# Optimization experiments

Hardware: AMD Instinct MI355X
Metric: run time of the kernel (lower is better)

Reference implementation:

```python
import jax, jax.numpy as jnp
import numpy as np

B, S, D, H, NL = 4, 1024, 512, 8, 2
DFF = 4 * D
EPS = 1e-5


def _layernorm(x, g, b):
    m = x.mean(-1, keepdims=True)
    v = ((x - m) ** 2).mean(-1, keepdims=True)
    return (x - m) / jnp.sqrt(v + EPS) * g + b


def _forward(x, Wq, bq, Wk, bk, Wv, bv, Wo, bo, W1, b1, W2, b2, ln1_g, ln1_b, ln2_g, ln2_b):
    Bn, Sn, Dn = x.shape
    Nl, Hh = Wq.shape[0], Wq.shape[1]
    dk = Dn // Hh  # scaling uses dmodel//h even though heads are full-width (faithful to SDPA)
    for i in range(Nl):
        # per-head full-width projections: each head maps dmodel -> dmodel
        q = jnp.einsum('bsd,hed->bhse', x, Wq[i]) + bq[i][:, None, :]
        k = jnp.einsum('bsd,hed->bhse', x, Wk[i]) + bk[i][:, None, :]
        v = jnp.einsum('bsd,hed->bhse', x, Wv[i]) + bv[i][:, None, :]
        scores = jnp.einsum('bhse,bhte->bhst', q, k) / jnp.sqrt(jnp.asarray(dk, x.dtype))
        attn = jax.nn.softmax(scores, axis=-1)
        heads = jnp.einsum('bhst,bhte->bhse', attn, v)          # [B,H,S,D]
        cat = heads.transpose(0, 2, 1, 3).reshape(Bn, Sn, Hh * Dn)  # concat heads -> [B,S,H*D]
        mha_out = cat @ Wo[i].T + bo[i]
        x = _layernorm(x + mha_out, ln1_g[i], ln1_b[i])
        ff = jax.nn.relu(x @ W1[i].T + b1[i]) @ W2[i].T + b2[i]
        x = _layernorm(x + ff, ln2_g[i], ln2_b[i])
    return x


def setup_inputs() -> dict:
    key = jax.random.key(0)
    ks = jax.random.split(key, 12)
    def w(k, shape, fan_in):
        return (jax.random.normal(k, shape, jnp.float32) / np.sqrt(fan_in)).astype(jnp.float32)
    inp = {
        'x': jax.random.normal(ks[0], (B, S, D), jnp.float32),
        'Wq': w(ks[1], (NL, H, D, D), D), 'bq': jnp.zeros((NL, H, D), jnp.float32),
        'Wk': w(ks[2], (NL, H, D, D), D), 'bk': jnp.zeros((NL, H, D), jnp.float32),
        'Wv': w(ks[3], (NL, H, D, D), D), 'bv': jnp.zeros((NL, H, D), jnp.float32),
        'Wo': w(ks[4], (NL, D, H * D), H * D), 'bo': jnp.zeros((NL, D), jnp.float32),
        'W1': w(ks[5], (NL, DFF, D), D), 'b1': jnp.zeros((NL, DFF), jnp.float32),
        'W2': w(ks[6], (NL, D, DFF), DFF), 'b2': jnp.zeros((NL, D), jnp.float32),
        'ln1_g': jnp.ones((NL, D), jnp.float32), 'ln1_b': jnp.zeros((NL, D), jnp.float32),
        'ln2_g': jnp.ones((NL, D), jnp.float32), 'ln2_b': jnp.zeros((NL, D), jnp.float32),
    }
    return inp


def reference(x, Wq, bq, Wk, bk, Wv, bv, Wo, bo, W1, b1, W2, b2, ln1_g, ln1_b, ln2_g, ln2_b):
    return _forward(x, Wq, bq, Wk, bk, Wv, bv, Wo, bo, W1, b1, W2, b2, ln1_g, ln1_b, ln2_g, ln2_b)
```

## Files before the change

### kernel.cpp

```cpp
#include <hip/hip_runtime.h>
#include <cstdint>
#include <cstddef>

#define NB 4
#define NS 1024
#define ND 512
#define NH 8
#define NLAYER 2
#define NDFF 2048

typedef __attribute__((ext_vector_type(8))) short short8;
typedef __attribute__((ext_vector_type(4))) float f32x4;
typedef __attribute__((ext_vector_type(4))) unsigned short u16x4;
typedef unsigned short u16;
typedef long long ll;

__device__ __forceinline__ float b2f(u16 u) {
  union { unsigned int i; float f; } x; x.i = ((unsigned int)u) << 16; return x.f;
}
__device__ __forceinline__ u16 f2b(float f) {
  union { float f; unsigned int i; } x; x.f = f;
  return (u16)((x.i + 0x7FFF + ((x.i >> 16) & 1)) >> 16);
}

struct Zm { int div; ll hi, lo; };
__device__ __forceinline__ ll zoff(Zm m, int z) {
  return (ll)(z / m.div) * m.hi + (ll)(z % m.div) * m.lo;
}

enum { F_BF16 = 1, F_RELU = 2, F_BCOL = 4, F_BROW = 8, F_RESID = 16 };

__device__ __forceinline__ void load_lds16(const void* g, void* s) {
  __builtin_amdgcn_global_load_lds(
      (const __attribute__((address_space(1))) void*)(uintptr_t)g,
      (__attribute__((address_space(3))) void*)(uint32_t)(uintptr_t)s, 16, 0, 0);
}

#define MFMA16(d, a, b) \
  asm volatile("v_mfma_f32_16x16x32_bf16 %0, %1, %2, %0" : "+v"(d) : "v"(a), "v"(b))

__global__ void __launch_bounds__(512, 2)
gemm8(const u16* __restrict__ A, int lda, Zm za,
      const u16* __restrict__ Bw, int ldb, Zm zb,
      const u16* __restrict__ Bw2, const float* __restrict__ bias2, int zsplit,
      void* __restrict__ Cv, int ldc, Zm zc,
      const float* __restrict__ bias, Zm zbias,
      const float* __restrict__ resid,
      float scale, int K, int flags)
{
  __shared__ __align__(16) char smem[2][65536];

  const int gx = gridDim.x, gy = gridDim.y;
  int id = (blockIdx.z * gy + blockIdx.y) * gx + blockIdx.x;
  const int nwg = gx * gy * (int)gridDim.z;
  if ((nwg & 7) == 0) id = (id & 7) * (nwg >> 3) + (id >> 3);
  const int bx = id % gx;
  const int rest = id / gx;
  const int by = rest % gy;
  const int z0 = rest / gy;

  int zB = z0;
  const u16* Bsel = Bw;
  const float* bsel = bias;
  if (z0 >= zsplit) { Bsel = Bw2; bsel = bias2; zB = z0 - zsplit; }

  A    += zoff(za, z0);
  Bsel += zoff(zb, zB);

  const int bm = by * 256, bn = bx * 256;
  const int t = threadIdx.x;
  const int w = t >> 6, lane = t & 63;
  const int wr = w >> 2, wc = w & 3;

  const int swcol = (((t & 7) ^ ((t >> 3) & 7)) << 3);
  const u16* srcA = A    + (size_t)(bm + (t >> 3)) * lda + swcol;
  const u16* srcB = Bsel + (size_t)(bn + (t >> 3)) * ldb + swcol;
  char* const sbase = (char*)smem;
  const int wofs = w << 10;

  auto STAGE_A = [&](int kt) {
    const ll kofs = (ll)kt << 6;
    char* d0 = sbase + ((kt & 1) << 16);
#pragma unroll
    for (int h = 0; h < 2; ++h)
#pragma unroll
      for (int i = 0; i < 2; ++i)
        load_lds16(srcA + (size_t)(h * 128 + i * 64) * lda + kofs,
                   d0 + h * 16384 + i * 8192 + wofs);
  };
  auto STAGE_B = [&](int kt) {
    const ll kofs = (ll)kt << 6;
    char* d0 = sbase + ((kt & 1) << 16) + 32768;
#pragma unroll
    for (int h = 0; h < 2; ++h)
#pragma unroll
      for (int i = 0; i < 2; ++i)
        load_lds16(srcB + (size_t)(h * 128 + i * 64) * ldb + kofs,
                   d0 + h * 16384 + i * 8192 + wofs);
  };

  const int fr  = lane & 15;
  const int khi = lane >> 4;
  const int swz = (fr & 7) << 3;
  const int colk0 = (khi * 8) ^ swz;
  const int colk1 = (32 + khi * 8) ^ swz;
  const int bbase = (wc & 1) * 64;

  f32x4 acc[8][4];
#pragma unroll
  for (int i = 0; i < 8; ++i)
#pragma unroll
    for (int j = 0; j < 4; ++j) acc[i][j] = (f32x4){0.f, 0.f, 0.f, 0.f};

  const int nt = K >> 6;
  STAGE_A(0);
  STAGE_B(0);
  __syncthreads();

  for (int T = 0; T < nt; ++T) {
    const char* bufp = sbase + ((T & 1) << 16);
    const u16* sA = (const u16*)(bufp + wr * 16384);
    const u16* sB = (const u16*)(bufp + 32768 + (wc >> 1) * 16384);
    const bool more = (T + 1) < nt;

    short8 bfr[4][2];
#pragma unroll
    for (int ni = 0; ni < 4; ++ni) {
      const int rb = (bbase + ni * 16 + fr) * 64;
      bfr[ni][0] = *(const short8*)(sB + rb + colk0);
      bfr[ni][1] = *(const short8*)(sB + rb + colk1);
    }

#pragma unroll
    for (int q = 0; q < 4; ++q) {
      short8 afr[2][2];
#pragma unroll
      for (int sub = 0; sub < 2; ++sub) {
        const int ra = (q * 32 + sub * 16 + fr) * 64;
        afr[sub][0] = *(const short8*)(sA + ra + colk0);
        afr[sub][1] = *(const short8*)(sA + ra + colk1);
      }
      if (q == 0 && more) STAGE_A(T + 1);
      if (q == 1 && more) STAGE_B(T + 1);
      __builtin_amdgcn_s_setprio(1);
#pragma unroll
      for (int sub = 0; sub < 2; ++sub)
#pragma unroll
        for (int ni = 0; ni < 4; ++ni) {
          MFMA16(acc[q * 2 + sub][ni], afr[sub][0], bfr[ni][0]);
          MFMA16(acc[q * 2 + sub][ni], afr[sub][1], bfr[ni][1]);
        }
      __builtin_amdgcn_s_setprio(0);
    }
    __syncthreads();
  }

  asm volatile("s_nop 7\n\ts_nop 7" ::: "memory");

  const ll co = zoff(zc, z0);
  const float* bz = (flags & (F_BCOL | F_BROW)) ? bsel + zoff(zbias, zB) : nullptr;
  const int r0 = (lane >> 4) << 2;
  const int c0 = lane & 15;
#pragma unroll
  for (int mi = 0; mi < 8; ++mi) {
#pragma unroll
    for (int ni = 0; ni < 4; ++ni) {
#pragma unroll
      for (int r = 0; r < 4; ++r) {
        const int grow = bm + wr * 128 + mi * 16 + r0 + r;
        const int gcol = bn + wc * 64 + ni * 16 + c0;
        float v = acc[mi][ni][r] * scale;
        if (flags & F_BCOL) v += bz[gcol];
        if (flags & F_BROW) v += bz[grow];
        if (flags & F_RELU) v = fmaxf(v, 0.f);
        if (flags & F_RESID) v += resid[(size_t)grow * ldc + gcol];
        const ll idx = co + (ll)grow * ldc + gcol;
        if (flags & F_BF16) ((u16*)Cv)[idx] = f2b(v);
        else                ((float*)Cv)[idx] = v;
      }
    }
  }
}

__global__ void __launch_bounds__(256)
softmax_rows(u16* __restrict__ sc)
{
  const int t = threadIdx.x, w = t >> 6, lane = t & 63;
  u16* p = sc + ((ll)blockIdx.x * 4 + w) * 1024 + lane * 16;
  short8 a = *(const short8*)p;
  short8 b = *(const short8*)(p + 8);
  float v[16];
#pragma unroll
  for (int j = 0; j < 8; ++j) { v[j] = b2f((u16)a[j]); v[8 + j] = b2f((u16)b[j]); }
  float mx = v[0];
#pragma unroll
  for (int j = 1; j < 16; ++j) mx = fmaxf(mx, v[j]);
#pragma unroll
  for (int o = 32; o >= 1; o >>= 1) mx = fmaxf(mx, __shfl_xor(mx, o));
  float s = 0.f;
#pragma unroll
  for (int j = 0; j < 16; ++j) { v[j] = __expf(v[j] - mx); s += v[j]; }
#pragma unroll
  for (int o = 32; o >= 1; o >>= 1) s += __shfl_xor(s, o);
  const float inv = 1.f / s;
  short8 oa, ob;
#pragma unroll
  for (int j = 0; j < 8; ++j) {
    oa[j] = (short)f2b(v[j] * inv);
    ob[j] = (short)f2b(v[8 + j] * inv);
  }
  *(short8*)p = oa;
  *(short8*)(p + 8) = ob;
}

__global__ void __launch_bounds__(256)
ln_red(const float* __restrict__ parts, int np, ll pstride,
       const float* __restrict__ bias, const float* __restrict__ resid,
       const float* __restrict__ g, const float* __restrict__ be,
       float* __restrict__ xout, u16* __restrict__ xbout)
{
  const int t = threadIdx.x, w = t >> 6, lane = t & 63;
  const ll row = (ll)blockIdx.x * 4 + w;
  const ll base = row * ND + lane * 8;
  float v[8];
  *(f32x4*)(v)     = *(const f32x4*)(resid + base);
  *(f32x4*)(v + 4) = *(const f32x4*)(resid + base + 4);
#pragma unroll
  for (int j = 0; j < 8; ++j) v[j] += bias[lane * 8 + j];
  for (int pIdx = 0; pIdx < np; ++pIdx) {
    const float* pp = parts + pIdx * pstride + base;
    f32x4 a0 = *(const f32x4*)(pp);
    f32x4 a1 = *(const f32x4*)(pp + 4);
    v[0] += a0.x; v[1] += a0.y; v[2] += a0.z; v[3] += a0.w;
    v[4] += a1.x; v[5] += a1.y; v[6] += a1.z; v[7] += a1.w;
  }
  float s = 0.f, q = 0.f;
#pragma unroll
  for (int j = 0; j < 8; ++j) { s += v[j]; q += v[j] * v[j]; }
#pragma unroll
  for (int o = 32; o >= 1; o >>= 1) { s += __shfl_xor(s, o); q += __shfl_xor(q, o); }
  const float mean = s * (1.f / ND);
  const float var  = q * (1.f / ND) - mean * mean;
  const float inv  = 1.f / sqrtf(var + 1e-5f);
#pragma unroll
  for (int j = 0; j < 8; ++j) {
    const int c = lane * 8 + j;
    const float y = (v[j] - mean) * inv * g[c] + be[c];
    xout[row * ND + c] = y;
    xbout[row * ND + c] = f2b(y);
  }
}

struct CvtJobs { const float* src[7]; u16* dst[7]; ll n[7]; };

__global__ void __launch_bounds__(256)
cvt7(CvtJobs j)
{
  const int z = blockIdx.y;
  const ll i = ((ll)blockIdx.x * 256 + threadIdx.x) * 4;
  if (i >= j.n[z]) return;
  f32x4 v = *(const f32x4*)(j.src[z] + i);
  u16x4 o;
  o.x = f2b(v.x); o.y = f2b(v.y); o.z = f2b(v.z); o.w = f2b(v.w);
  *(u16x4*)(j.dst[z] + i) = o;
}

extern "C" void kernel_launch(void* const* d_in, const int* in_sizes, int n_in,
                              void* d_out, int out_size, void* d_ws, size_t ws_size,
                              hipStream_t stream)
{
  (void)in_sizes; (void)n_in; (void)out_size; (void)ws_size;
  const float* x_in = (const float*)d_in[0];
  const float* Wq = (const float*)d_in[1];  const float* bq = (const float*)d_in[2];
  const float* Wk = (const float*)d_in[3];  const float* bk = (const float*)d_in[4];
  const float* Wv = (const float*)d_in[5];  const float* bv = (const float*)d_in[6];
  const float* Wo = (const float*)d_in[7];  const float* bo = (const float*)d_in[8];
  const float* W1 = (const float*)d_in[9];  const float* b1 = (const float*)d_in[10];
  const float* W2 = (const float*)d_in[11]; const float* b2 = (const float*)d_in[12];
  const float* ln1g = (const float*)d_in[13]; const float* ln1b = (const float*)d_in[14];
  const float* ln2g = (const float*)d_in[15]; const float* ln2b = (const float*)d_in[16];

  char* p = (char*)d_ws;
  auto alloc = [&](ll bytes) { char* r = p; p += (bytes + 255) & ~(ll)255; return r; };
  const ll nWq = (ll)NLAYER * NH * ND * ND;
  const ll nWo = (ll)NLAYER * ND * NH * ND;
  const ll nW1 = (ll)NLAYER * NDFF * ND;
  const ll nX  = (ll)NB * NS * ND;

  u16* wq_b = (u16*)alloc(nWq * 2);
  u16* wk_b = (u16*)alloc(nWq * 2);
  u16* wv_b = (u16*)alloc(nWq * 2);
  u16* wo_b = (u16*)alloc(nWo * 2);
  u16* w1_b = (u16*)alloc(nW1 * 2);
  u16* w2_b = (u16*)alloc(nW1 * 2);
  u16* xb   = (u16*)alloc(nX * 2);
  u16* qb   = (u16*)alloc((ll)NH * NB * NS * ND * 2);
  u16* kb   = (u16*)alloc((ll)NH * NB * NS * ND * 2);
  u16* vT   = (u16*)alloc((ll)NH * NB * ND * NS * 2);
  u16* scb  = (u16*)alloc((ll)NB * NH * NS * NS * 2);
  u16* cat = kb;
  u16* ffh = qb;
  float* parts = (float*)scb;

  CvtJobs cj;
  cj.src[0] = Wq; cj.dst[0] = wq_b; cj.n[0] = nWq;
  cj.src[1] = Wk; cj.dst[1] = wk_b; cj.n[1] = nWq;
  cj.src[2] = Wv; cj.dst[2] = wv_b; cj.n[2] = nWq;
  cj.src[3] = Wo; cj.dst[3] = wo_b; cj.n[3] = nWo;
  cj.src[4] = W1; cj.dst[4] = w1_b; cj.n[4] = nW1;
  cj.src[5] = W2; cj.dst[5] = w2_b; cj.n[5] = nW1;
  cj.src[6] = x_in; cj.dst[6] = xb; cj.n[6] = nX;
  cvt7<<<dim3((unsigned)((nWq / 4 + 255) / 256), 7), 256, 0, stream>>>(cj);

  float* xf = (float*)d_out;
  const Zm Z0{1, 0, 0};
  const ll PSTR = (ll)NB * NS * ND;
  const int ZINF = 1 << 30;

  for (int i = 0; i < NLAYER; ++i) {
    const float* resid1 = (i == 0) ? x_in : xf;
    const ll woff = (ll)i * NH * ND * ND;

    gemm8<<<dim3(ND/256, (NB*NS)/256, 2*NH), 512, 0, stream>>>(
        xb, ND, Z0,
        wq_b + woff, ND, Zm{1, (ll)ND * ND, 0},
        wk_b + woff, bk + (ll)i * NH * ND, NH,
        qb, ND, Zm{1, (ll)NB * NS * ND, 0},
        bq + (ll)i * NH * ND, Zm{1, ND, 0}, nullptr, 1.f, ND, F_BF16 | F_BCOL);

    gemm8<<<dim3(NS/256, ND/256, NH*NB), 512, 0, stream>>>(
        wv_b + woff, ND, Zm{NB, (ll)ND * ND, 0},
        xb, ND, Zm{NB, 0, (ll)NS * ND},
        xb, nullptr, ZINF,
        vT, NS, Zm{1, (ll)ND * NS, 0},
        bv + (ll)i * NH * ND, Zm{NB, ND, 0}, nullptr, 1.f, ND, F_BF16 | F_BROW);

    gemm8<<<dim3(NS/256, NS/256, NH*NB), 512, 0, stream>>>(
        qb, ND, Zm{NB, (ll)NB * NS * ND, (ll)NS * ND},
        kb, ND, Zm{NB, (ll)NB * NS * ND, (ll)NS * ND},
        kb, nullptr, ZINF,
        scb, NS, Zm{1, (ll)NS * NS, 0},
        nullptr, Z0, nullptr, 0.125f, ND, F_BF16);

    softmax_rows<<<dim3(NB * NH * NS / 4), 256, 0, stream>>>(scb);

    gemm8<<<dim3(ND/256, NS/256, NH*NB), 512, 0, stream>>>(
        scb, NS, Zm{1, (ll)NS * NS, 0},
        vT, NS, Zm{1, (ll)ND * NS, 0},
        vT, nullptr, ZINF,
        cat, NH * ND, Zm{NB, (ll)ND, (ll)NS * NH * ND},
        nullptr, Z0, nullptr, 1.f, NS, F_BF16);

    gemm8<<<dim3(ND/256, (NB*NS)/256, 8), 512, 0, stream>>>(
        cat, NH * ND, Zm{1, 512, 0},
        wo_b + (ll)i * ND * NH * ND, NH * ND, Zm{1, 512, 0},
        wo_b, nullptr, ZINF,
        parts, ND, Zm{1, PSTR, 0},
        nullptr, Z0, nullptr, 1.f, 512, 0);

    ln_red<<<dim3(NB * NS / 4), 256, 0, stream>>>(
        parts, 8, PSTR, bo + (ll)i * ND, resid1,
        ln1g + (ll)i * ND, ln1b + (ll)i * ND, xf, xb);

    gemm8<<<dim3(NDFF/256, (NB*NS)/256, 1), 512, 0, stream>>>(
        xb, ND, Z0,
        w1_b + (ll)i * NDFF * ND, ND, Z0,
        w1_b, nullptr, ZINF,
        ffh, NDFF, Z0,
        b1 + (ll)i * NDFF, Z0, nullptr, 1.f, ND, F_BF16 | F_BCOL | F_RELU);

    gemm8<<<dim3(ND/256, (NB*NS)/256, 8), 512, 0, stream>>>(
        ffh, NDFF, Zm{1, 256, 0},
        w2_b + (ll)i * ND * NDFF, NDFF, Zm{1, 256, 0},
        w2_b, nullptr, ZINF,
        parts, ND, Zm{1, PSTR, 0},
        nullptr, Z0, nullptr, 1.f, 256, 0);

    ln_red<<<dim3(NB * NS / 4), 256, 0, stream>>>(
        parts, 8, PSTR, b2 + (ll)i * ND, xf,
        ln2g + (ll)i * ND, ln2b + (ll)i * ND, xf, xb);
  }
}
```

Measured before the change: 754.4 us.

## Split GEMM tile staging into finer parts with vmcnt waits and barriers

Restructures the GEMM main loop's double-buffered global-to-LDS staging. Loads are issued in eight smaller parts, interleaved between the four MFMA quarter-phases, and ordered to match the sequence in which rows are consumed. The full __syncthreads is replaced by explicit s_waitcnt vmcnt counts and s_barrier calls, so waves wait only for the portion of the next tile they need. This adds more barriers per iteration, and correctness depends on the vmcnt counts matching the load ordering, so a miscount could cause a race or a stall.

New measurement: 762.2 us. About the same (+1.0%).

```diff
diff --git a/kernel.cpp b/kernel.cpp
--- a/kernel.cpp
+++ b/kernel.cpp
@@ -38,6 +38,23 @@
 
 #define MFMA16(d, a, b) \
   asm volatile("v_mfma_f32_16x16x32_bf16 %0, %1, %2, %0" : "+v"(d) : "v"(a), "v"(b))
+
+#define READ_A(q, afr) do {                                         \
+  _Pragma("unroll") for (int sub = 0; sub < 2; ++sub) {             \
+    const int ra = ((q) * 32 + sub * 16 + fr) * 64;                 \
+    (afr)[sub][0] = *(const short8*)(sA + ra + colk0);              \
+    (afr)[sub][1] = *(const short8*)(sA + ra + colk1); } } while (0)
+
+#define MFMAQ(q, afr) do {                                          \
+  __builtin_amdgcn_s_setprio(1);                                    \
+  _Pragma("unroll") for (int sub = 0; sub < 2; ++sub)               \
+    _Pragma("unroll") for (int ni = 0; ni < 4; ++ni) {              \
+      MFMA16(acc[(q) * 2 + sub][ni], (afr)[sub][0], bfr[ni][0]);    \
+      MFMA16(acc[(q) * 2 + sub][ni], (afr)[sub][1], bfr[ni][1]); }  \
+  __builtin_amdgcn_s_setprio(0); } while (0)
+
+#define WAITVM(n) asm volatile("s_waitcnt vmcnt(" #n ")" ::: "memory")
+#define BAR() __builtin_amdgcn_s_barrier()
 
 __global__ void __launch_bounds__(512, 2)
 gemm8(const u16* __restrict__ A, int lda, Zm za,
@@ -78,25 +95,13 @@
   char* const sbase = (char*)smem;
   const int wofs = w << 10;
 
-  auto STAGE_A = [&](int kt) {
-    const ll kofs = (ll)kt << 6;
-    char* d0 = sbase + ((kt & 1) << 16);
-#pragma unroll
-    for (int h = 0; h < 2; ++h)
-#pragma unroll
-      for (int i = 0; i < 2; ++i)
-        load_lds16(srcA + (size_t)(h * 128 + i * 64) * lda + kofs,
-                   d0 + h * 16384 + i * 8192 + wofs);
-  };
-  auto STAGE_B = [&](int kt) {
-    const ll kofs = (ll)kt << 6;
-    char* d0 = sbase + ((kt & 1) << 16) + 32768;
-#pragma unroll
-    for (int h = 0; h < 2; ++h)
-#pragma unroll
-      for (int i = 0; i < 2; ++i)
-        load_lds16(srcB + (size_t)(h * 128 + i * 64) * ldb + kofs,
-                   d0 + h * 16384 + i * 8192 + wofs);
+  auto STG = [&](int kt, int tensor, int part) {
+    const int h = part >> 1, i2 = part & 1;
+    const u16* src = tensor ? srcB : srcA;
+    const int ld = tensor ? ldb : lda;
+    load_lds16(src + (size_t)(h * 128 + i2 * 64) * ld + ((ll)kt << 6),
+               sbase + ((kt & 1) << 16) + tensor * 32768 +
+                   h * 16384 + i2 * 8192 + wofs);
   };
 
   const int fr  = lane & 15;
@@ -113,15 +118,19 @@
     for (int j = 0; j < 4; ++j) acc[i][j] = (f32x4){0.f, 0.f, 0.f, 0.f};
 
   const int nt = K >> 6;
-  STAGE_A(0);
-  STAGE_B(0);
-  __syncthreads();
+
+  STG(0, 0, 0); STG(0, 0, 2);
+  STG(0, 1, 0); STG(0, 1, 1); STG(0, 1, 2); STG(0, 1, 3);
+  STG(0, 0, 1); STG(0, 0, 3);
 
   for (int T = 0; T < nt; ++T) {
+    const bool more = (T + 1) < nt;
     const char* bufp = sbase + ((T & 1) << 16);
     const u16* sA = (const u16*)(bufp + wr * 16384);
     const u16* sB = (const u16*)(bufp + 32768 + (wc >> 1) * 16384);
-    const bool more = (T + 1) < nt;
+
+    WAITVM(2);
+    BAR();
 
     short8 bfr[4][2];
 #pragma unroll
@@ -130,29 +139,32 @@
       bfr[ni][0] = *(const short8*)(sB + rb + colk0);
       bfr[ni][1] = *(const short8*)(sB + rb + colk1);
     }
-
-#pragma unroll
-    for (int q = 0; q < 4; ++q) {
-      short8 afr[2][2];
-#pragma unroll
-      for (int sub = 0; sub < 2; ++sub) {
-        const int ra = (q * 32 + sub * 16 + fr) * 64;
-        afr[sub][0] = *(const short8*)(sA + ra + colk0);
-        afr[sub][1] = *(const short8*)(sA + ra + colk1);
-      }
-      if (q == 0 && more) STAGE_A(T + 1);
-      if (q == 1 && more) STAGE_B(T + 1);
-      __builtin_amdgcn_s_setprio(1);
-#pragma unroll
-      for (int sub = 0; sub < 2; ++sub)
-#pragma unroll
-        for (int ni = 0; ni < 4; ++ni) {
-          MFMA16(acc[q * 2 + sub][ni], afr[sub][0], bfr[ni][0]);
-          MFMA16(acc[q * 2 + sub][ni], afr[sub][1], bfr[ni][1]);
-        }
-      __builtin_amdgcn_s_setprio(0);
-    }
-    __syncthreads();
+    short8 af0[2][2];
+    READ_A(0, af0);
+    if (more) { STG(T + 1, 0, 0); STG(T + 1, 0, 2); }
+    BAR();
+    MFMAQ(0, af0);
+
+    short8 af1[2][2];
+    READ_A(1, af1);
+    if (more) { STG(T + 1, 1, 0); STG(T + 1, 1, 1); }
+    BAR();
+    MFMAQ(1, af1);
+
+    if (more) { WAITVM(4); } else { WAITVM(0); }
+    BAR();
+
+    short8 af2[2][2];
+    READ_A(2, af2);
+    if (more) { STG(T + 1, 1, 2); STG(T + 1, 1, 3); }
+    BAR();
+    MFMAQ(2, af2);
+
+    short8 af3[2][2];
+    READ_A(3, af3);
+    if (more) { STG(T + 1, 0, 1); STG(T + 1, 0, 3); }
+    BAR();
+    MFMAQ(3, af3);
   }
 
   asm volatile("s_nop 7\n\ts_nop 7" ::: "memory");
```
